# Optimization experiments

Measured on AMD Instinct MI355X. Metric: run time of the kernel, lower is better.

## Reference

```python
import jax, jax.numpy as jnp
import numpy as np

B = 4096      # number of boards
H = 256       # n_hidden
SCALE = 0.0625  # 1/sqrt(H)
N_POLICY = 1858


def setup_inputs() -> dict:
    key = jax.random.key(0)
    ks = jax.random.split(key, 10)
    w_s = 1.0 / 16.0  # keep activations well-scaled
    return {
        "x": jax.random.normal(ks[0], (B * 64, H), jnp.float32),
        "w1": jax.random.normal(ks[1], (H, H), jnp.float32) * w_s,
        "b1": jax.random.normal(ks[2], (H,), jnp.float32) * w_s,
        "w2": jax.random.normal(ks[3], (H, H), jnp.float32) * w_s,
        "b2": jax.random.normal(ks[4], (H,), jnp.float32) * w_s,
        "w3": jax.random.normal(ks[5], (H, H), jnp.float32) * w_s,
        "b3": jax.random.normal(ks[6], (H,), jnp.float32) * w_s,
        "w4": jax.random.normal(ks[7], (4, H), jnp.float32) * w_s,
        "gather_idx": jax.random.randint(ks[8], (N_POLICY,), 0, 4288, jnp.int32),
    }


def reference(x, w1, b1, w2, b2, w3, b3, w4, gather_idx):
    out = jax.nn.relu(x @ w1.T + b1)                      # (B*64, H)
    q = (out @ w2.T + b2).reshape(-1, 64, H)              # (B, 64, H)
    k = (out @ w3.T + b3).reshape(-1, 64, H)              # (B, 64, H)
    logits = jnp.einsum("bqh,bkh->bqk", q, k) * SCALE     # (B, 64, 64)

    # promotion offsets from 8th-rank keys
    promo_keys = k[:, 56:64, :]                           # (B, 8, H)
    offs = jnp.einsum("bsh,ph->bps", promo_keys, w4)      # (B, 4, 8)
    offs = offs[:, :3, :] + offs[:, 3:4, :]               # (B, 3, 8) q/r/b + knight base
    off24 = jnp.transpose(offs, (0, 2, 1)).reshape(-1, 1, 24)  # (B,1,24) piece-fastest

    # knight promotion move logits: rank7 -> rank8 block
    n_promo = logits[:, 48:56, 56:64].reshape(-1, 64, 1)  # (B, 64, 1)
    n_promo = jnp.broadcast_to(n_promo, (n_promo.shape[0], 64, 3)).reshape(-1, 8, 24)

    promo = (off24 + n_promo).reshape(-1, 3, 64)          # (B, 3, 64)

    full = jnp.concatenate([logits, promo], axis=1).reshape(-1, 4288)  # (B, 4288)
    return jnp.take(full, gather_idx, axis=1)             # (B, 1858)
```

## Files before the change

### kernel.cpp

```cpp
#include <hip/hip_runtime.h>


typedef __bf16 bf16_t;
typedef __bf16 bf16x8 __attribute__((ext_vector_type(8)));
typedef float  f32x4  __attribute__((ext_vector_type(4)));

#define PSCALE 0.0625f
#define NPOL   1858
#define MFMA(a,b,c) __builtin_amdgcn_mfma_f32_16x16x32_bf16(a, b, c, 0, 0, 0)

__global__ void prep_weights(const float* __restrict__ w1,
                             const float* __restrict__ w2,
                             const float* __restrict__ w3,
                             bf16_t* __restrict__ wf) {
    int i = blockIdx.x * 256 + threadIdx.x;
    int which = i >> 16;
    int r = i & 65535;
    int j    = r & 7;
    int lane = (r >> 3) & 63;
    int t    = (r >> 9) & 7;
    int n    = (r >> 12) & 15;
    const float* w = (which == 0) ? w1 : (which == 1 ? w2 : w3);
    int row = n * 16 + (lane & 15);
    int col = t * 32 + (lane >> 4) * 8 + j;
    wf[i] = (bf16_t)w[row * 256 + col];
}

template <bool USE_WS>
__device__ __forceinline__ bf16x8 wfrag(const bf16_t* __restrict__ wl,
                                        const float* __restrict__ w,
                                        int n, int t, int lane) {
    if (USE_WS) {
        return *(const bf16x8*)(wl + (((n * 8 + t) * 64 + lane) << 3));
    } else {
        int l15 = lane & 15, quad = lane >> 4;
        const float* p = w + (n * 16 + l15) * 256 + t * 32 + quad * 8;
        f32x4 lo = *(const f32x4*)p;
        f32x4 hi = *(const f32x4*)(p + 4);
        bf16x8 v;
        v[0] = (bf16_t)lo[0]; v[1] = (bf16_t)lo[1];
        v[2] = (bf16_t)lo[2]; v[3] = (bf16_t)lo[3];
        v[4] = (bf16_t)hi[0]; v[5] = (bf16_t)hi[1];
        v[6] = (bf16_t)hi[2]; v[7] = (bf16_t)hi[3];
        return v;
    }
}

__device__ __forceinline__ int ks_off(int row, int col) {
    return ((row << 9) + (col << 1)) ^ ((row & 7) << 4);
}

__device__ __forceinline__ bf16x8 cvt8(const float* __restrict__ p) {
    f32x4 lo = *(const f32x4*)p;
    f32x4 hi = *(const f32x4*)(p + 4);
    bf16x8 v;
    v[0] = (bf16_t)lo[0]; v[1] = (bf16_t)lo[1];
    v[2] = (bf16_t)lo[2]; v[3] = (bf16_t)lo[3];
    v[4] = (bf16_t)hi[0]; v[5] = (bf16_t)hi[1];
    v[6] = (bf16_t)hi[2]; v[7] = (bf16_t)hi[3];
    return v;
}

template <bool USE_WS, bool RELU>
__device__ __forceinline__ void layer2b(const bf16x8* inA, const bf16x8* inB,
                                        const bf16_t* __restrict__ wl,
                                        const float* __restrict__ wraw,
                                        const float* __restrict__ bias,
                                        unsigned char* __restrict__ u_lds,
                                        int lane, int quad, int l15, int R) {
    bf16x8 wA[4], wB[4];
    #pragma unroll
    for (int t = 0; t < 4; ++t)
        wA[t] = wfrag<USE_WS>(wl, wraw, 0, t, lane);

    #pragma unroll
    for (int n = 0; n < 16; ++n) {
        #pragma unroll
        for (int t = 0; t < 4; ++t)
            wB[t] = wfrag<USE_WS>(wl, wraw, n, 4 + t, lane);

        f32x4 aA0 = {0.f,0.f,0.f,0.f}, aA1 = {0.f,0.f,0.f,0.f};
        f32x4 aB0 = {0.f,0.f,0.f,0.f}, aB1 = {0.f,0.f,0.f,0.f};
        aA0 = MFMA(inA[0], wA[0], aA0);  aB0 = MFMA(inB[0], wA[0], aB0);
        aA1 = MFMA(inA[1], wA[1], aA1);  aB1 = MFMA(inB[1], wA[1], aB1);
        aA0 = MFMA(inA[2], wA[2], aA0);  aB0 = MFMA(inB[2], wA[2], aB0);
        aA1 = MFMA(inA[3], wA[3], aA1);  aB1 = MFMA(inB[3], wA[3], aB1);

        if (n < 15) {
            #pragma unroll
            for (int t = 0; t < 4; ++t)
                wA[t] = wfrag<USE_WS>(wl, wraw, n + 1, t, lane);
        }

        aA0 = MFMA(inA[4], wB[0], aA0);  aB0 = MFMA(inB[4], wB[0], aB0);
        aA1 = MFMA(inA[5], wB[1], aA1);  aB1 = MFMA(inB[5], wB[1], aB1);
        aA0 = MFMA(inA[6], wB[2], aA0);  aB0 = MFMA(inB[6], wB[2], aB0);
        aA1 = MFMA(inA[7], wB[3], aA1);  aB1 = MFMA(inB[7], wB[3], aB1);

        f32x4 sA = aA0 + aA1, sB = aB0 + aB1;
        float bv = bias[n * 16 + l15];
        #pragma unroll
        for (int r2 = 0; r2 < 4; ++r2) {
            int off = ks_off(R + quad * 4 + r2, n * 16 + l15);
            float vA = sA[r2] + bv, vB = sB[r2] + bv;
            if (RELU) { vA = fmaxf(vA, 0.f); vB = fmaxf(vB, 0.f); }
            *(bf16_t*)(u_lds + off)         = (bf16_t)vA;
            *(bf16_t*)(u_lds + 32768 + off) = (bf16_t)vB;
        }
    }
}

template <bool USE_WS>
__global__ __launch_bounds__(256, 2)
void policy_main(const float* __restrict__ x,
                 const bf16_t* __restrict__ wf,
                 const float* __restrict__ w1,
                 const float* __restrict__ w2,
                 const float* __restrict__ w3,
                 const float* __restrict__ b1,
                 const float* __restrict__ b2,
                 const float* __restrict__ b3,
                 const float* __restrict__ w4,
                 const int*   __restrict__ gidx,
                 float* __restrict__ out,
                 int nbat) {
    __shared__ __align__(16) unsigned char u_lds[2 * 32768];
    __shared__ __align__(16) bf16_t qscr[4][2][16 * 40];
    __shared__ float promoLDS[2][4][8];
    __shared__ float patchLDS[2][8][8];

    const int tid  = threadIdx.x;
    const int lane = tid & 63;
    const int wv   = tid >> 6;
    const int quad = lane >> 4;
    const int l15  = lane & 15;
    const int R    = wv * 16;

    const int bat0 = blockIdx.x * 2;
    const bool has1 = (bat0 + 1) < nbat;
    const int bat1 = has1 ? bat0 + 1 : bat0;

    bf16x8 xaA[8], xaB[8];
    {
        const float* xr0 = x + ((size_t)bat0 * 64 + R + l15) * 256;
        const float* xr1 = x + ((size_t)bat1 * 64 + R + l15) * 256;
        #pragma unroll
        for (int t = 0; t < 8; ++t) {
            xaA[t] = cvt8(xr0 + t * 32 + quad * 8);
            xaB[t] = cvt8(xr1 + t * 32 + quad * 8);
        }
    }

    layer2b<USE_WS, true>(xaA, xaB, wf, w1, b1, u_lds, lane, quad, l15, R);
    bf16x8 oaA[8], oaB[8];
    #pragma unroll
    for (int t = 0; t < 8; ++t) {
        int off = ks_off(R + l15, t * 32 + quad * 8);
        oaA[t] = *(const bf16x8*)(u_lds + off);
        oaB[t] = *(const bf16x8*)(u_lds + 32768 + off);
    }

    layer2b<USE_WS, false>(oaA, oaB, wf + 2 * 65536, w3, b3, u_lds,
                           lane, quad, l15, R);

    __syncthreads();

    f32x4 laA[4], laB[4];
    #pragma unroll
    for (int n = 0; n < 4; ++n) {
        laA[n] = (f32x4){0.f,0.f,0.f,0.f};
        laB[n] = (f32x4){0.f,0.f,0.f,0.f};
    }
    {
        const bf16_t* wl = wf + 65536;
        bf16_t* qsA = &qscr[wv][0][0];
        bf16_t* qsB = &qscr[wv][1][0];
        bf16x8 wA[4], wB[4];
        #pragma unroll
        for (int t = 0; t < 4; ++t)
            wA[t] = wfrag<USE_WS>(wl, w2, 0, t, lane);

        #pragma unroll
        for (int t8 = 0; t8 < 8; ++t8) {
            const int n0 = 2 * t8, n1 = n0 + 1;

            #pragma unroll
            for (int t = 0; t < 4; ++t)
                wB[t] = wfrag<USE_WS>(wl, w2, n0, 4 + t, lane);
            {
                f32x4 cA0 = {0.f,0.f,0.f,0.f}, cA1 = {0.f,0.f,0.f,0.f};
                f32x4 cB0 = {0.f,0.f,0.f,0.f}, cB1 = {0.f,0.f,0.f,0.f};
                cA0 = MFMA(oaA[0], wA[0], cA0);  cB0 = MFMA(oaB[0], wA[0], cB0);
                cA1 = MFMA(oaA[1], wA[1], cA1);  cB1 = MFMA(oaB[1], wA[1], cB1);
                cA0 = MFMA(oaA[2], wA[2], cA0);  cB0 = MFMA(oaB[2], wA[2], cB0);
                cA1 = MFMA(oaA[3], wA[3], cA1);  cB1 = MFMA(oaB[3], wA[3], cB1);
                #pragma unroll
                for (int t = 0; t < 4; ++t)
                    wA[t] = wfrag<USE_WS>(wl, w2, n1, t, lane);
                cA0 = MFMA(oaA[4], wB[0], cA0);  cB0 = MFMA(oaB[4], wB[0], cB0);
                cA1 = MFMA(oaA[5], wB[1], cA1);  cB1 = MFMA(oaB[5], wB[1], cB1);
                cA0 = MFMA(oaA[6], wB[2], cA0);  cB0 = MFMA(oaB[6], wB[2], cB0);
                cA1 = MFMA(oaA[7], wB[3], cA1);  cB1 = MFMA(oaB[7], wB[3], cB1);
                f32x4 sA = cA0 + cA1, sB = cB0 + cB1;
                float bv = b2[n0 * 16 + l15];
                #pragma unroll
                for (int r2 = 0; r2 < 4; ++r2) {
                    int qo = (quad * 4 + r2) * 40 + l15;
                    qsA[qo] = (bf16_t)(sA[r2] + bv);
                    qsB[qo] = (bf16_t)(sB[r2] + bv);
                }
            }

            #pragma unroll
            for (int t = 0; t < 4; ++t)
                wB[t] = wfrag<USE_WS>(wl, w2, n1, 4 + t, lane);
            {
                f32x4 cA0 = {0.f,0.f,0.f,0.f}, cA1 = {0.f,0.f,0.f,0.f};
                f32x4 cB0 = {0.f,0.f,0.f,0.f}, cB1 = {0.f,0.f,0.f,0.f};
                cA0 = MFMA(oaA[0], wA[0], cA0);  cB0 = MFMA(oaB[0], wA[0], cB0);
                cA1 = MFMA(oaA[1], wA[1], cA1);  cB1 = MFMA(oaB[1], wA[1], cB1);
                cA0 = MFMA(oaA[2], wA[2], cA0);  cB0 = MFMA(oaB[2], wA[2], cB0);
                cA1 = MFMA(oaA[3], wA[3], cA1);  cB1 = MFMA(oaB[3], wA[3], cB1);
                if (t8 < 7) {
                    #pragma unroll
                    for (int t = 0; t < 4; ++t)
                        wA[t] = wfrag<USE_WS>(wl, w2, n0 + 2, t, lane);
                }
                cA0 = MFMA(oaA[4], wB[0], cA0);  cB0 = MFMA(oaB[4], wB[0], cB0);
                cA1 = MFMA(oaA[5], wB[1], cA1);  cB1 = MFMA(oaB[5], wB[1], cB1);
                cA0 = MFMA(oaA[6], wB[2], cA0);  cB0 = MFMA(oaB[6], wB[2], cB0);
                cA1 = MFMA(oaA[7], wB[3], cA1);  cB1 = MFMA(oaB[7], wB[3], cB1);
                f32x4 sA = cA0 + cA1, sB = cB0 + cB1;
                float bv = b2[n1 * 16 + l15];
                #pragma unroll
                for (int r2 = 0; r2 < 4; ++r2) {
                    int qo = (quad * 4 + r2) * 40 + 16 + l15;
                    qsA[qo] = (bf16_t)(sA[r2] + bv);
                    qsB[qo] = (bf16_t)(sB[r2] + bv);
                }
            }

            bf16x8 qaA = *(const bf16x8*)(qsA + l15 * 40 + quad * 8);
            bf16x8 qaB = *(const bf16x8*)(qsB + l15 * 40 + quad * 8);
            #pragma unroll
            for (int np = 0; np < 4; ++np) {
                int ko = ks_off(np * 16 + l15, t8 * 32 + quad * 8);
                bf16x8 kA = *(const bf16x8*)(u_lds + ko);
                bf16x8 kB = *(const bf16x8*)(u_lds + 32768 + ko);
                laA[np] = MFMA(qaA, kA, laA[np]);
                laB[np] = MFMA(qaB, kB, laB[np]);
            }
        }
    }

    {
        int s = lane >> 3, seg = lane & 7;
        const float* wrow = w4 + wv * 256;
        #pragma unroll
        for (int b = 0; b < 2; ++b) {
            const unsigned char* kb = u_lds + b * 32768;
            float p = 0.f;
            #pragma unroll
            for (int m = 0; m < 4; ++m) {
                bf16x8 kv = *(const bf16x8*)(kb + ks_off(56 + s, seg * 32 + m * 8));
                f32x4 wa = *(const f32x4*)(wrow + seg * 32 + m * 8);
                f32x4 wb = *(const f32x4*)(wrow + seg * 32 + m * 8 + 4);
                p += (float)kv[0] * wa[0] + (float)kv[1] * wa[1]
                   + (float)kv[2] * wa[2] + (float)kv[3] * wa[3]
                   + (float)kv[4] * wb[0] + (float)kv[5] * wb[1]
                   + (float)kv[6] * wb[2] + (float)kv[7] * wb[3];
            }
            p += __shfl_down(p, 4);
            p += __shfl_down(p, 2);
            p += __shfl_down(p, 1);
            if (seg == 0) promoLDS[b][wv][s] = p;
        }
    }

    if (wv == 3 && quad < 2 && l15 >= 8) {
        #pragma unroll
        for (int r2 = 0; r2 < 4; ++r2) {
            patchLDS[0][quad * 4 + r2][l15 - 8] = laA[3][r2] * PSCALE;
            patchLDS[1][quad * 4 + r2][l15 - 8] = laB[3][r2] * PSCALE;
        }
    }

    __syncthreads();

    float* fb0 = (float*)u_lds;
    float* fb1 = (float*)(u_lds + 32768);
    #pragma unroll
    for (int n = 0; n < 4; ++n) {
        #pragma unroll
        for (int r2 = 0; r2 < 4; ++r2) {
            int idx = (R + quad * 4 + r2) * 64 + n * 16 + l15;
            fb0[idx] = laA[n][r2] * PSCALE;
            fb1[idx] = laB[n][r2] * PSCALE;
        }
    }

    if (tid < 192) {
        int u = tid >> 6, vv = tid & 63;
        int mm = u * 64 + vv;
        int r_ = mm / 24, c_ = mm - r_ * 24;
        int c3 = c_ / 3, cp = c_ - c3 * 3;
        fb0[(64 + u) * 64 + vv] =
            promoLDS[0][cp][c3] + promoLDS[0][3][c3] + patchLDS[0][r_][c3];
        fb1[(64 + u) * 64 + vv] =
            promoLDS[1][cp][c3] + promoLDS[1][3][c3] + patchLDS[1][r_][c3];
    }

    __syncthreads();

    {
        float* orow0 = out + (size_t)bat0 * NPOL;
        float* orow1 = out + (size_t)(bat0 + 1) * NPOL;
        int   idxv[8];
        float v0[8], v1[8];
        #pragma unroll
        for (int i = 0; i < 8; ++i) {
            int g = tid + i * 256;
            idxv[i] = (g < NPOL) ? gidx[g] : 0;
        }
        #pragma unroll
        for (int i = 0; i < 8; ++i) {
            v0[i] = fb0[idxv[i]];
            v1[i] = fb1[idxv[i]];
        }
        #pragma unroll
        for (int i = 0; i < 8; ++i) {
            int g = tid + i * 256;
            if (g < NPOL) {
                orow0[g] = v0[i];
                if (has1) orow1[g] = v1[i];
            }
        }
    }
}

extern "C" void kernel_launch(void* const* d_in, const int* in_sizes, int n_in,
                              void* d_out, int out_size, void* d_ws, size_t ws_size,
                              hipStream_t stream) {
    const float* x    = (const float*)d_in[0];
    const float* w1   = (const float*)d_in[1];
    const float* b1   = (const float*)d_in[2];
    const float* w2   = (const float*)d_in[3];
    const float* b2   = (const float*)d_in[4];
    const float* w3   = (const float*)d_in[5];
    const float* b3   = (const float*)d_in[6];
    const float* w4   = (const float*)d_in[7];
    const int*   gidx = (const int*)d_in[8];
    float* out = (float*)d_out;
    bf16_t* wf = (bf16_t*)d_ws;

    int nbat = in_sizes[0] / (64 * 256);
    int nblk = (nbat + 1) / 2;
    const size_t ws_needed = (size_t)3 * 65536 * sizeof(bf16_t);

    if (ws_size >= ws_needed) {
        prep_weights<<<768, 256, 0, stream>>>(w1, w2, w3, wf);
        policy_main<true><<<nblk, 256, 0, stream>>>(
            x, wf, w1, w2, w3, b1, b2, b3, w4, gidx, out, nbat);
    } else {
        policy_main<false><<<nblk, 256, 0, stream>>>(
            x, wf, w1, w2, w3, b1, b2, b3, w4, gidx, out, nbat);
    }
}
```

Before: 523.5 us.

## Fold W2ᵀW3 into a single bilinear matrix and skip the K projection

Precomputes M = W2ᵀW3 plus the bias and promotion vectors (b2·W3, W2ᵀb3, w4·W3) in prep kernels. The fused kernel then computes logits as out·M·outᵀ plus rank-one bias terms, and takes promotion offsets directly from the layer-1 output. This removes one of the two 256x256 projections per board, dropping the separate K GEMM. The trade-off is a serial 256-step reduction per element in the prep kernels and a different bf16 rounding path, since M is quantized to bf16.

```diff
diff --git a/kernel.cpp b/kernel.cpp
--- a/kernel.cpp
+++ b/kernel.cpp
@@ -9,28 +9,69 @@
 #define NPOL   1858
 #define MFMA(a,b,c) __builtin_amdgcn_mfma_f32_16x16x32_bf16(a, b, c, 0, 0, 0)
 
-__global__ void prep_weights(const float* __restrict__ w1,
-                             const float* __restrict__ w2,
-                             const float* __restrict__ w3,
-                             bf16_t* __restrict__ wf) {
+
+__global__ void prep_w1(const float* __restrict__ w1, bf16_t* __restrict__ wfA) {
     int i = blockIdx.x * 256 + threadIdx.x;
-    int which = i >> 16;
-    int r = i & 65535;
-    int j    = r & 7;
-    int lane = (r >> 3) & 63;
-    int t    = (r >> 9) & 7;
-    int n    = (r >> 12) & 15;
-    const float* w = (which == 0) ? w1 : (which == 1 ? w2 : w3);
+    int j = i & 7, lane = (i >> 3) & 63, t = (i >> 9) & 7, n = (i >> 12) & 15;
     int row = n * 16 + (lane & 15);
     int col = t * 32 + (lane >> 4) * 8 + j;
-    wf[i] = (bf16_t)w[row * 256 + col];
-}
+    wfA[i] = (bf16_t)w1[row * 256 + col];
+}
+
+__global__ void prep_mat(const float* __restrict__ w2,
+                         const float* __restrict__ w3,
+                         bf16_t* __restrict__ wfM) {
+    int m1 = blockIdx.x, m2 = threadIdx.x;
+    float acc = 0.f;
+    #pragma unroll 8
+    for (int h = 0; h < 256; ++h)
+        acc += w2[h * 256 + m1] * w3[h * 256 + m2];
+    int t = m1 >> 5, quad = (m1 >> 3) & 3, j = m1 & 7;
+    int n = m2 >> 4, l15 = m2 & 15;
+    wfM[(((n * 8 + t) * 64) + (quad * 16 + l15)) * 8 + j] = (bf16_t)acc;
+}
+
+__global__ void prep_vecs(const float* __restrict__ w2,
+                          const float* __restrict__ w3,
+                          const float* __restrict__ b2,
+                          const float* __restrict__ b3,
+                          const float* __restrict__ w4,
+                          float* __restrict__ flt) {
+    int m = threadIdx.x;
+    float c2 = 0.f, vv = 0.f, p0 = 0.f, p1 = 0.f, p2 = 0.f, p3 = 0.f;
+    for (int h = 0; h < 256; ++h) {
+        float w3h = w3[h * 256 + m];
+        c2 += b2[h] * w3h;
+        p0 += w4[h] * w3h;
+        p1 += w4[256 + h] * w3h;
+        p2 += w4[512 + h] * w3h;
+        p3 += w4[768 + h] * w3h;
+        vv += w2[h * 256 + m] * b3[h];
+    }
+    flt[m]        = c2;
+    flt[256 + m]  = vv;
+    flt[512 + m]  = p0;
+    flt[768 + m]  = p1;
+    flt[1024 + m] = p2;
+    flt[1280 + m] = p3;
+    if (m < 4) {
+        float pb = 0.f;
+        for (int h = 0; h < 256; ++h) pb += w4[m * 256 + h] * b3[h];
+        flt[1536 + m] = pb;
+    }
+    if (m == 0) {
+        float s = 0.f;
+        for (int h = 0; h < 256; ++h) s += b2[h] * b3[h];
+        flt[1540] = s;
+    }
+}
+
 
 template <bool USE_WS>
 __device__ __forceinline__ bf16x8 wfrag(const bf16_t* __restrict__ wl,
                                         const float* __restrict__ w,
                                         int n, int t, int lane) {
-    if (USE_WS) {
+    if constexpr (USE_WS) {
         return *(const bf16x8*)(wl + (((n * 8 + t) * 64 + lane) << 3));
     } else {
         int l15 = lane & 15, quad = lane >> 4;
@@ -106,6 +147,252 @@
             if (RELU) { vA = fmaxf(vA, 0.f); vB = fmaxf(vB, 0.f); }
             *(bf16_t*)(u_lds + off)         = (bf16_t)vA;
             *(bf16_t*)(u_lds + 32768 + off) = (bf16_t)vB;
+        }
+    }
+}
+
+__global__ __launch_bounds__(256, 2)
+void policy_fused(const float* __restrict__ x,
+                  const bf16_t* __restrict__ wfA,
+                  const bf16_t* __restrict__ wfM,
+                  const float* __restrict__ flt,
+                  const float* __restrict__ b1,
+                  const int*   __restrict__ gidx,
+                  float* __restrict__ out,
+                  int nbat) {
+    __shared__ __align__(16) unsigned char u_lds[2 * 32768];
+    __shared__ __align__(16) bf16_t qscr[4][2][16 * 40];
+    __shared__ float promoLDS[2][4][8];
+    __shared__ float patchLDS[2][8][8];
+
+    const int tid  = threadIdx.x;
+    const int lane = tid & 63;
+    const int wv   = tid >> 6;
+    const int quad = lane >> 4;
+    const int l15  = lane & 15;
+    const int R    = wv * 16;
+
+    const int bat0 = blockIdx.x * 2;
+    const bool has1 = (bat0 + 1) < nbat;
+    const int bat1 = has1 ? bat0 + 1 : bat0;
+
+    bf16x8 xaA[8], xaB[8];
+    {
+        const float* xr0 = x + ((size_t)bat0 * 64 + R + l15) * 256;
+        const float* xr1 = x + ((size_t)bat1 * 64 + R + l15) * 256;
+        #pragma unroll
+        for (int t = 0; t < 8; ++t) {
+            xaA[t] = cvt8(xr0 + t * 32 + quad * 8);
+            xaB[t] = cvt8(xr1 + t * 32 + quad * 8);
+        }
+    }
+
+    layer2b<true, true>(xaA, xaB, wfA, nullptr, b1, u_lds, lane, quad, l15, R);
+    bf16x8 oaA[8], oaB[8];
+    #pragma unroll
+    for (int t = 0; t < 8; ++t) {
+        int off = ks_off(R + l15, t * 32 + quad * 8);
+        oaA[t] = *(const bf16x8*)(u_lds + off);
+        oaB[t] = *(const bf16x8*)(u_lds + 32768 + off);
+    }
+
+    float qbA = flt[1540], qbB = qbA;
+    {
+        const float* vvec = flt + 256;
+        #pragma unroll
+        for (int t = 0; t < 8; ++t) {
+            f32x4 va = *(const f32x4*)(vvec + t * 32 + quad * 8);
+            f32x4 vb = *(const f32x4*)(vvec + t * 32 + quad * 8 + 4);
+            qbA += (float)oaA[t][0]*va[0] + (float)oaA[t][1]*va[1]
+                 + (float)oaA[t][2]*va[2] + (float)oaA[t][3]*va[3]
+                 + (float)oaA[t][4]*vb[0] + (float)oaA[t][5]*vb[1]
+                 + (float)oaA[t][6]*vb[2] + (float)oaA[t][7]*vb[3];
+            qbB += (float)oaB[t][0]*va[0] + (float)oaB[t][1]*va[1]
+                 + (float)oaB[t][2]*va[2] + (float)oaB[t][3]*va[3]
+                 + (float)oaB[t][4]*vb[0] + (float)oaB[t][5]*vb[1]
+                 + (float)oaB[t][6]*vb[2] + (float)oaB[t][7]*vb[3];
+        }
+        qbA += __shfl_xor(qbA, 16);  qbA += __shfl_xor(qbA, 32);
+        qbB += __shfl_xor(qbB, 16);  qbB += __shfl_xor(qbB, 32);
+    }
+
+    __syncthreads();
+
+    f32x4 laA[4], laB[4];
+    #pragma unroll
+    for (int n = 0; n < 4; ++n) {
+        laA[n] = (f32x4){0.f,0.f,0.f,0.f};
+        laB[n] = (f32x4){0.f,0.f,0.f,0.f};
+    }
+    {
+        bf16_t* qsA = &qscr[wv][0][0];
+        bf16_t* qsB = &qscr[wv][1][0];
+        bf16x8 wA[4], wB[4];
+        #pragma unroll
+        for (int t = 0; t < 4; ++t)
+            wA[t] = wfrag<true>(wfM, nullptr, 0, t, lane);
+
+        #pragma unroll
+        for (int t8 = 0; t8 < 8; ++t8) {
+            const int n0 = 2 * t8, n1 = n0 + 1;
+
+            #pragma unroll
+            for (int t = 0; t < 4; ++t)
+                wB[t] = wfrag<true>(wfM, nullptr, n0, 4 + t, lane);
+            {
+                f32x4 cA0 = {0.f,0.f,0.f,0.f}, cA1 = {0.f,0.f,0.f,0.f};
+                f32x4 cB0 = {0.f,0.f,0.f,0.f}, cB1 = {0.f,0.f,0.f,0.f};
+                cA0 = MFMA(oaA[0], wA[0], cA0);  cB0 = MFMA(oaB[0], wA[0], cB0);
+                cA1 = MFMA(oaA[1], wA[1], cA1);  cB1 = MFMA(oaB[1], wA[1], cB1);
+                cA0 = MFMA(oaA[2], wA[2], cA0);  cB0 = MFMA(oaB[2], wA[2], cB0);
+                cA1 = MFMA(oaA[3], wA[3], cA1);  cB1 = MFMA(oaB[3], wA[3], cB1);
+                #pragma unroll
+                for (int t = 0; t < 4; ++t)
+                    wA[t] = wfrag<true>(wfM, nullptr, n1, t, lane);
+                cA0 = MFMA(oaA[4], wB[0], cA0);  cB0 = MFMA(oaB[4], wB[0], cB0);
+                cA1 = MFMA(oaA[5], wB[1], cA1);  cB1 = MFMA(oaB[5], wB[1], cB1);
+                cA0 = MFMA(oaA[6], wB[2], cA0);  cB0 = MFMA(oaB[6], wB[2], cB0);
+                cA1 = MFMA(oaA[7], wB[3], cA1);  cB1 = MFMA(oaB[7], wB[3], cB1);
+                f32x4 sA = cA0 + cA1, sB = cB0 + cB1;
+                float bv = flt[n0 * 16 + l15];
+                #pragma unroll
+                for (int r2 = 0; r2 < 4; ++r2) {
+                    int qo = (quad * 4 + r2) * 40 + l15;
+                    qsA[qo] = (bf16_t)(sA[r2] + bv);
+                    qsB[qo] = (bf16_t)(sB[r2] + bv);
+                }
+            }
+
+            #pragma unroll
+            for (int t = 0; t < 4; ++t)
+                wB[t] = wfrag<true>(wfM, nullptr, n1, 4 + t, lane);
+            {
+                f32x4 cA0 = {0.f,0.f,0.f,0.f}, cA1 = {0.f,0.f,0.f,0.f};
+                f32x4 cB0 = {0.f,0.f,0.f,0.f}, cB1 = {0.f,0.f,0.f,0.f};
+                cA0 = MFMA(oaA[0], wA[0], cA0);  cB0 = MFMA(oaB[0], wA[0], cB0);
+                cA1 = MFMA(oaA[1], wA[1], cA1);  cB1 = MFMA(oaB[1], wA[1], cB1);
+                cA0 = MFMA(oaA[2], wA[2], cA0);  cB0 = MFMA(oaB[2], wA[2], cB0);
+                cA1 = MFMA(oaA[3], wA[3], cA1);  cB1 = MFMA(oaB[3], wA[3], cB1);
+                if (t8 < 7) {
+                    #pragma unroll
+                    for (int t = 0; t < 4; ++t)
+                        wA[t] = wfrag<true>(wfM, nullptr, n0 + 2, t, lane);
+                }
+                cA0 = MFMA(oaA[4], wB[0], cA0);  cB0 = MFMA(oaB[4], wB[0], cB0);
+                cA1 = MFMA(oaA[5], wB[1], cA1);  cB1 = MFMA(oaB[5], wB[1], cB1);
+                cA0 = MFMA(oaA[6], wB[2], cA0);  cB0 = MFMA(oaB[6], wB[2], cB0);
+                cA1 = MFMA(oaA[7], wB[3], cA1);  cB1 = MFMA(oaB[7], wB[3], cB1);
+                f32x4 sA = cA0 + cA1, sB = cB0 + cB1;
+                float bv = flt[n1 * 16 + l15];
+                #pragma unroll
+                for (int r2 = 0; r2 < 4; ++r2) {
+                    int qo = (quad * 4 + r2) * 40 + 16 + l15;
+                    qsA[qo] = (bf16_t)(sA[r2] + bv);
+                    qsB[qo] = (bf16_t)(sB[r2] + bv);
+                }
+            }
+
+            bf16x8 qaA = *(const bf16x8*)(qsA + l15 * 40 + quad * 8);
+            bf16x8 qaB = *(const bf16x8*)(qsB + l15 * 40 + quad * 8);
+            #pragma unroll
+            for (int np = 0; np < 4; ++np) {
+                int ko = ks_off(np * 16 + l15, t8 * 32 + quad * 8);
+                bf16x8 kA = *(const bf16x8*)(u_lds + ko);
+                bf16x8 kB = *(const bf16x8*)(u_lds + 32768 + ko);
+                laA[np] = MFMA(qaA, kA, laA[np]);
+                laB[np] = MFMA(qaB, kB, laB[np]);
+            }
+        }
+    }
+
+    float qbra[4], qbrb[4];
+    #pragma unroll
+    for (int r2 = 0; r2 < 4; ++r2) {
+        qbra[r2] = __shfl(qbA, quad * 4 + r2);
+        qbrb[r2] = __shfl(qbB, quad * 4 + r2);
+    }
+
+    {
+        int s = lane >> 3, seg = lane & 7;
+        const float* wrow = flt + 512 + wv * 256;
+        #pragma unroll
+        for (int b = 0; b < 2; ++b) {
+            const unsigned char* kb = u_lds + b * 32768;
+            float p = 0.f;
+            #pragma unroll
+            for (int m = 0; m < 4; ++m) {
+                bf16x8 kv = *(const bf16x8*)(kb + ks_off(56 + s, seg * 32 + m * 8));
+                f32x4 wa = *(const f32x4*)(wrow + seg * 32 + m * 8);
+                f32x4 wb = *(const f32x4*)(wrow + seg * 32 + m * 8 + 4);
+                p += (float)kv[0] * wa[0] + (float)kv[1] * wa[1]
+                   + (float)kv[2] * wa[2] + (float)kv[3] * wa[3]
+                   + (float)kv[4] * wb[0] + (float)kv[5] * wb[1]
+                   + (float)kv[6] * wb[2] + (float)kv[7] * wb[3];
+            }
+            p += __shfl_down(p, 4);
+            p += __shfl_down(p, 2);
+            p += __shfl_down(p, 1);
+            if (seg == 0) promoLDS[b][wv][s] = p + flt[1536 + wv];
+        }
+    }
+
+    if (wv == 3 && quad < 2 && l15 >= 8) {
+        #pragma unroll
+        for (int r2 = 0; r2 < 4; ++r2) {
+            patchLDS[0][quad * 4 + r2][l15 - 8] = (laA[3][r2] + qbra[r2]) * PSCALE;
+            patchLDS[1][quad * 4 + r2][l15 - 8] = (laB[3][r2] + qbrb[r2]) * PSCALE;
+        }
+    }
+
+    __syncthreads();
+
+    float* fb0 = (float*)u_lds;
+    float* fb1 = (float*)(u_lds + 32768);
+    #pragma unroll
+    for (int n = 0; n < 4; ++n) {
+        #pragma unroll
+        for (int r2 = 0; r2 < 4; ++r2) {
+            int idx = (R + quad * 4 + r2) * 64 + n * 16 + l15;
+            fb0[idx] = (laA[n][r2] + qbra[r2]) * PSCALE;
+            fb1[idx] = (laB[n][r2] + qbrb[r2]) * PSCALE;
+        }
+    }
+
+    if (tid < 192) {
+        int u = tid >> 6, vv2 = tid & 63;
+        int mm = u * 64 + vv2;
+        int r_ = mm / 24, c_ = mm - r_ * 24;
+        int c3 = c_ / 3, cp = c_ - c3 * 3;
+        fb0[(64 + u) * 64 + vv2] =
+            promoLDS[0][cp][c3] + promoLDS[0][3][c3] + patchLDS[0][r_][c3];
+        fb1[(64 + u) * 64 + vv2] =
+            promoLDS[1][cp][c3] + promoLDS[1][3][c3] + patchLDS[1][r_][c3];
+    }
+
+    __syncthreads();
+
+    {
+        float* orow0 = out + (size_t)bat0 * NPOL;
+        float* orow1 = out + (size_t)(bat0 + 1) * NPOL;
+        int   idxv[8];
+        float v0[8], v1[8];
+        #pragma unroll
+        for (int i = 0; i < 8; ++i) {
+            int g = tid + i * 256;
+            idxv[i] = (g < NPOL) ? gidx[g] : 0;
+        }
+        #pragma unroll
+        for (int i = 0; i < 8; ++i) {
+            v0[i] = fb0[idxv[i]];
+            v1[i] = fb1[idxv[i]];
+        }
+        #pragma unroll
+        for (int i = 0; i < 8; ++i) {
+            int g = tid + i * 256;
+            if (g < NPOL) {
+                orow0[g] = v0[i];
+                if (has1) orow1[g] = v1[i];
+            }
         }
     }
 }
@@ -183,7 +470,6 @@
         #pragma unroll
         for (int t8 = 0; t8 < 8; ++t8) {
             const int n0 = 2 * t8, n1 = n0 + 1;
-
             #pragma unroll
             for (int t = 0; t < 4; ++t)
                 wB[t] = wfrag<USE_WS>(wl, w2, n0, 4 + t, lane);
@@ -210,7 +496,6 @@
                     qsB[qo] = (bf16_t)(sB[r2] + bv);
                 }
             }
-
             #pragma unroll
             for (int t = 0; t < 4; ++t)
                 wB[t] = wfrag<USE_WS>(wl, w2, n1, 4 + t, lane);
@@ -239,7 +524,6 @@
                     qsB[qo] = (bf16_t)(sB[r2] + bv);
                 }
             }
-
             bf16x8 qaA = *(const bf16x8*)(qsA + l15 * 40 + quad * 8);
             bf16x8 qaB = *(const bf16x8*)(qsB + l15 * 40 + quad * 8);
             #pragma unroll
@@ -300,13 +584,13 @@
     }
 
     if (tid < 192) {
-        int u = tid >> 6, vv = tid & 63;
-        int mm = u * 64 + vv;
+        int u = tid >> 6, vv2 = tid & 63;
+        int mm = u * 64 + vv2;
         int r_ = mm / 24, c_ = mm - r_ * 24;
         int c3 = c_ / 3, cp = c_ - c3 * 3;
-        fb0[(64 + u) * 64 + vv] =
+        fb0[(64 + u) * 64 + vv2] =
             promoLDS[0][cp][c3] + promoLDS[0][3][c3] + patchLDS[0][r_][c3];
-        fb1[(64 + u) * 64 + vv] =
+        fb1[(64 + u) * 64 + vv2] =
             promoLDS[1][cp][c3] + promoLDS[1][3][c3] + patchLDS[1][r_][c3];
     }
 
@@ -351,18 +635,22 @@
     const float* w4   = (const float*)d_in[7];
     const int*   gidx = (const int*)d_in[8];
     float* out = (float*)d_out;
-    bf16_t* wf = (bf16_t*)d_ws;
 
     int nbat = in_sizes[0] / (64 * 256);
     int nblk = (nbat + 1) / 2;
-    const size_t ws_needed = (size_t)3 * 65536 * sizeof(bf16_t);
+    const size_t ws_needed = 262144 + 8192;
 
     if (ws_size >= ws_needed) {
-        prep_weights<<<768, 256, 0, stream>>>(w1, w2, w3, wf);
-        policy_main<true><<<nblk, 256, 0, stream>>>(
-            x, wf, w1, w2, w3, b1, b2, b3, w4, gidx, out, nbat);
+        bf16_t* wfA = (bf16_t*)d_ws;
+        bf16_t* wfM = wfA + 65536;
+        float*  flt = (float*)((char*)d_ws + 262144);
+        prep_w1  <<<256, 256, 0, stream>>>(w1, wfA);
+        prep_mat <<<256, 256, 0, stream>>>(w2, w3, wfM);
+        prep_vecs<<<1,   256, 0, stream>>>(w2, w3, b2, b3, w4, flt);
+        policy_fused<<<nblk, 256, 0, stream>>>(
+            x, wfA, wfM, flt, b1, gidx, out, nbat);
     } else {
         policy_main<false><<<nblk, 256, 0, stream>>>(
-            x, wf, w1, w2, w3, b1, b2, b3, w4, gidx, out, nbat);
-    }
-}
+            x, nullptr, w1, w2, w3, b1, b2, b3, w4, gidx, out, nbat);
+    }
+}
```

After: 501.4 us. 4.2% less time.
